# Kernel optimization log

Hardware: AMD Instinct MI355X
Metric: run time of the kernel (lower is better)

Reference implementation:

```python
import jax, jax.numpy as jnp
import numpy as np

N, E, IN, HID, H, L, G = 20000, 320000, 128, 64, 4, 3, 128

def setup_inputs() -> dict:
    key = jax.random.key(0)
    ks = jax.random.split(key, 14)
    x = jax.random.normal(ks[0], (N, IN), dtype=jnp.float32)
    edge_index = jax.random.randint(ks[1], (2, E), 0, N, dtype=jnp.int64)
    batch = jnp.sort(jax.random.randint(ks[2], (N,), 0, G, dtype=jnp.int64))
    s_in = 1.0 / np.sqrt(IN)
    s_h = 1.0 / np.sqrt(HID)
    lin_W = jax.random.normal(ks[3], (IN, HID), jnp.float32) * s_in
    lin_b = jax.random.normal(ks[4], (HID,), jnp.float32) * 0.02
    Wq = jax.random.normal(ks[5], (L, HID, H * HID), jnp.float32) * s_h
    bq = jax.random.normal(ks[6], (L, H * HID), jnp.float32) * 0.02
    Wk = jax.random.normal(ks[7], (L, HID, H * HID), jnp.float32) * s_h
    bk = jax.random.normal(ks[8], (L, H * HID), jnp.float32) * 0.02
    Wv = jax.random.normal(ks[9], (L, HID, H * HID), jnp.float32) * s_h
    bv = jax.random.normal(ks[10], (L, H * HID), jnp.float32) * 0.02
    Ws = jax.random.normal(ks[11], (L, HID, HID), jnp.float32) * s_h
    bs = jax.random.normal(ks[12], (L, HID), jnp.float32) * 0.02
    return {"x": x, "edge_index": edge_index, "batch": batch,
            "lin_W": lin_W, "lin_b": lin_b, "Wq": Wq, "bq": bq,
            "Wk": Wk, "bk": bk, "Wv": Wv, "bv": bv, "Ws": Ws, "bs": bs}

def _transformer_conv(h, src, dst, Wq, bq, Wk, bk, Wv, bv, Ws, bs):
    # PyG TransformerConv(hid, hid, heads=H, concat=False), beta=False, root_weight=True
    n = h.shape[0]
    C = HID  # per-head dim
    q = (h @ Wq + bq).reshape(n, H, C)
    k = (h @ Wk + bk).reshape(n, H, C)
    v = (h @ Wv + bv).reshape(n, H, C)
    # per-edge attention logits: q_i . k_j / sqrt(C), i=dst (target), j=src
    alpha = jnp.einsum('ehc,ehc->eh', q[dst], k[src]) * (1.0 / np.sqrt(C))  # [E,H]
    # segment softmax over edges grouped by target node
    amax = jax.ops.segment_max(alpha, dst, num_segments=n)  # [N,H]
    amax = jnp.where(jnp.isfinite(amax), amax, 0.0)
    ex = jnp.exp(alpha - amax[dst])
    denom = jax.ops.segment_sum(ex, dst, num_segments=n)
    a = ex / jnp.maximum(denom[dst], 1e-16)  # [E,H]
    msg = a[:, :, None] * v[src]  # [E,H,C]
    agg = jax.ops.segment_sum(msg.reshape(-1, H * C), dst, num_segments=n)
    out = agg.reshape(n, H, C).mean(axis=1)  # concat=False -> head mean
    return out + h @ Ws + bs  # root/skip connection

def reference(x, edge_index, batch, lin_W, lin_b, Wq, bq, Wk, bk, Wv, bv, Ws, bs):
    src, dst = edge_index[0], edge_index[1]
    h = x @ lin_W + lin_b  # [N, HID]; dropout inactive in eval
    for l in range(L):
        h = jax.nn.relu(_transformer_conv(h, src, dst, Wq[l], bq[l], Wk[l], bk[l],
                                          Wv[l], bv[l], Ws[l], bs[l]))
    # global_add_pool: sum node features per graph
    return jax.ops.segment_sum(h, batch, num_segments=G)  # [G, HID]
```

## Files before the change

### kernel.cpp

```cpp
#include <hip/hip_runtime.h>
#include <math.h>

#define N_NODES 20000
#define N_EDGES 320000
#define DIM_IN 128
#define HID 64
#define HEADS 4
#define LAYERS 3
#define GRAPHS 128
#define QKVS 832
#define QSS 320

typedef unsigned short ushort;
typedef ushort ushort8 __attribute__((ext_vector_type(8)));

__device__ __forceinline__ float bf2f(ushort u) {
    return __uint_as_float(((unsigned int)u) << 16);
}
__device__ __forceinline__ ushort f2bf(float f) {
    unsigned int b = __float_as_uint(f);
    return (ushort)((b + 0x7FFFu + ((b >> 16) & 1u)) >> 16);
}


__global__ void zero_kernel(int* __restrict__ p, int n) {
    int i = blockIdx.x * 256 + threadIdx.x;
    if (i < n) p[i] = 0;
}

__global__ void hist_kernel(const int* __restrict__ dst, int* __restrict__ counts, int n) {
    int e = blockIdx.x * 256 + threadIdx.x;
    if (e < n) atomicAdd(&counts[dst[e]], 1);
}

__global__ __launch_bounds__(1024) void scan_kernel(const int* __restrict__ counts,
                                                    int* __restrict__ offs,
                                                    int* __restrict__ cursor, int n) {
    __shared__ int wsum[16];
    __shared__ int wpre[17];
    int tid = threadIdx.x;
    int wave = tid >> 6, lane = tid & 63;
    int base = 0;
    int nchunks = (n + 1023) / 1024;
    for (int chunk = 0; chunk < nchunks; ++chunk) {
        int i = chunk * 1024 + tid;
        int v = (i < n) ? counts[i] : 0;
        int s = v;
#pragma unroll
        for (int off = 1; off < 64; off <<= 1) {
            int t = __shfl_up(s, off);
            if (lane >= off) s += t;
        }
        if (lane == 63) wsum[wave] = s;
        __syncthreads();
        if (tid < 16) {
            int w = wsum[tid];
            int ws = w;
#pragma unroll
            for (int off = 1; off < 16; off <<= 1) {
                int t = __shfl_up(ws, off);
                if (lane >= off) ws += t;
            }
            wpre[tid] = ws - w;
            if (tid == 15) wpre[16] = ws;
        }
        __syncthreads();
        int excl = base + (s - v) + wpre[wave];
        if (i < n) { offs[i] = excl; cursor[i] = excl; }
        base += wpre[16];
        __syncthreads();
    }
    if (tid == 0) offs[n] = base;
}

__global__ void scatter_kernel(const int* __restrict__ src, const int* __restrict__ dst,
                               int* __restrict__ cursor, int* __restrict__ csr, int n) {
    int e = blockIdx.x * 256 + threadIdx.x;
    if (e < n) {
        int d = dst[e];
        int pos = atomicAdd(&cursor[d], 1);
        csr[pos] = src[e];
    }
}


__global__ __launch_bounds__(256) void lin_kernel(const float* __restrict__ x,
                                                  const float* __restrict__ W,
                                                  const float* __restrict__ b,
                                                  float* __restrict__ h0) {
    __shared__ float xt[32][DIM_IN];
    int tx = threadIdx.x;
    int row0 = blockIdx.x * 32;
    for (int idx = tx; idx < 32 * DIM_IN; idx += 256) {
        int r = idx / DIM_IN, c = idx % DIM_IN;
        xt[r][c] = x[(size_t)(row0 + r) * DIM_IN + c];
    }
    __syncthreads();
    int col = tx & 63;
    int sub = tx >> 6;
    float acc[8];
#pragma unroll
    for (int r = 0; r < 8; ++r) acc[r] = 0.f;
    for (int k = 0; k < DIM_IN; k += 4) {
        float w0 = W[k * HID + col];
        float w1 = W[(k + 1) * HID + col];
        float w2 = W[(k + 2) * HID + col];
        float w3 = W[(k + 3) * HID + col];
#pragma unroll
        for (int r = 0; r < 8; ++r) {
            const float4 hv = *(const float4*)&xt[r * 4 + sub][k];
            acc[r] += hv.x * w0 + hv.y * w1 + hv.z * w2 + hv.w * w3;
        }
    }
    float bias = b[col];
#pragma unroll
    for (int r = 0; r < 8; ++r) {
        int row = row0 + r * 4 + sub;
        h0[(size_t)row * HID + col] = acc[r] + bias;
    }
}


__global__ __launch_bounds__(256) void proj_kernel(const float* __restrict__ h,
                                                   const float* __restrict__ Wq, const float* __restrict__ bq,
                                                   const float* __restrict__ Wk, const float* __restrict__ bk,
                                                   const float* __restrict__ Wv, const float* __restrict__ bv,
                                                   const float* __restrict__ Ws, const float* __restrict__ bs,
                                                   float* __restrict__ qs,
                                                   ushort* __restrict__ kvpack) {
    __shared__ float ht[16][HID];
    int tx = threadIdx.x;
    int row0 = blockIdx.x * 16;
    for (int idx = tx; idx < 16 * HID; idx += 256) {
        ht[idx >> 6][idx & 63] = h[(size_t)(row0 + (idx >> 6)) * HID + (idx & 63)];
    }
    __syncthreads();
    int j = blockIdx.y * 256 + tx;
    if (j >= QKVS) return;
    const float* W; int ld; float bias;
    if (j < 256)      { W = Wq + j;         ld = 256; bias = bq[j]; }
    else if (j < 512) { W = Wk + (j - 256); ld = 256; bias = bk[j - 256]; }
    else if (j < 768) { W = Wv + (j - 512); ld = 256; bias = bv[j - 512]; }
    else              { W = Ws + (j - 768); ld = 64;  bias = bs[j - 768]; }
    float acc[16];
#pragma unroll
    for (int r = 0; r < 16; ++r) acc[r] = 0.f;
    for (int k = 0; k < HID; k += 4) {
        float w0 = W[(size_t)k * ld];
        float w1 = W[(size_t)(k + 1) * ld];
        float w2 = W[(size_t)(k + 2) * ld];
        float w3 = W[(size_t)(k + 3) * ld];
#pragma unroll
        for (int r = 0; r < 16; ++r) {
            const float4 hv = *(const float4*)&ht[r][k];
            acc[r] += hv.x * w0 + hv.y * w1 + hv.z * w2 + hv.w * w3;
        }
    }
    if (j < 256) {
#pragma unroll
        for (int r = 0; r < 16; ++r)
            qs[(size_t)(row0 + r) * QSS + j] = acc[r] + bias;
    } else if (j < 768) {
        int ck = j - 256;
        int isv = ck >> 8;
        int ch = ck & 255;
        int hh = ch >> 6, c = ch & 63;
        int pos = ((hh * 16 + (c >> 2)) * 8) + isv * 4 + (c & 3);
#pragma unroll
        for (int r = 0; r < 16; ++r)
            kvpack[(size_t)(row0 + r) * 512 + pos] = f2bf(acc[r] + bias);
    } else {
#pragma unroll
        for (int r = 0; r < 16; ++r)
            qs[(size_t)(row0 + r) * QSS + 256 + (j - 768)] = acc[r] + bias;
    }
}


__global__ __launch_bounds__(256) void edge_kernel(const float* __restrict__ qs,
                                                   const ushort8* __restrict__ kvp,
                                                   const int* __restrict__ offs,
                                                   const int* __restrict__ csr,
                                                   float* __restrict__ hout) {
    int wave = threadIdx.x >> 6;
    int lane = threadIdx.x & 63;
    int node = blockIdx.x * 4 + wave;
    if (node >= N_NODES) return;
    int hh = lane >> 4;
    int cb = (lane & 15) * 4;

    const float* nb = qs + (size_t)node * QSS;
    float4 q = *(const float4*)(nb + hh * 64 + cb);

    float m = -INFINITY, l = 0.f;
    float4 acc = make_float4(0.f, 0.f, 0.f, 0.f);

    int e0 = offs[node], e1 = offs[node + 1];
    int cnt = e1 - e0;

    ushort8 cur = (ushort8)(0);
    ushort8 nxt = (ushort8)(0);
    if (cnt > 0) cur = kvp[(size_t)csr[e0] * 64 + lane];
    if (cnt > 1) nxt = kvp[(size_t)csr[e0 + 1] * 64 + lane];

    for (int i = 0; i < cnt; ++i) {
        ushort8 u = cur;
        cur = nxt;
        if (i + 2 < cnt) nxt = kvp[(size_t)csr[e0 + i + 2] * 64 + lane];

        float p = q.x * bf2f(u[0]) + q.y * bf2f(u[1]) + q.z * bf2f(u[2]) + q.w * bf2f(u[3]);
        p += __shfl_xor(p, 1);
        p += __shfl_xor(p, 2);
        p += __shfl_xor(p, 4);
        p += __shfl_xor(p, 8);
        float alpha = p * 0.125f;
        float nm = fmaxf(m, alpha);
        float sc = __expf(m - nm);
        float pe = __expf(alpha - nm);
        l = l * sc + pe;
        acc.x = acc.x * sc + pe * bf2f(u[4]);
        acc.y = acc.y * sc + pe * bf2f(u[5]);
        acc.z = acc.z * sc + pe * bf2f(u[6]);
        acc.w = acc.w * sc + pe * bf2f(u[7]);
        m = nm;
    }

    float inv = (l > 0.f) ? (1.f / l) : 0.f;
    float4 r;
    r.x = acc.x * inv;
    r.y = acc.y * inv;
    r.z = acc.z * inv;
    r.w = acc.w * inv;
    r.x += __shfl_xor(r.x, 16); r.x += __shfl_xor(r.x, 32);
    r.y += __shfl_xor(r.y, 16); r.y += __shfl_xor(r.y, 32);
    r.z += __shfl_xor(r.z, 16); r.z += __shfl_xor(r.z, 32);
    r.w += __shfl_xor(r.w, 16); r.w += __shfl_xor(r.w, 32);

    if (hh == 0) {
        float4 s = *(const float4*)(nb + 256 + cb);
        float4 o;
        o.x = fmaxf(r.x * 0.25f + s.x, 0.f);
        o.y = fmaxf(r.y * 0.25f + s.y, 0.f);
        o.z = fmaxf(r.z * 0.25f + s.z, 0.f);
        o.w = fmaxf(r.w * 0.25f + s.w, 0.f);
        *(float4*)(hout + (size_t)node * HID + cb) = o;
    }
}


__global__ __launch_bounds__(256) void pool_kernel(const float* __restrict__ h,
                                                   const int* __restrict__ batch,
                                                   float* __restrict__ out) {
    int g = blockIdx.x;
    int lo = 0, hi = N_NODES;
    while (lo < hi) { int mid = (lo + hi) >> 1; if (batch[mid] < g) lo = mid + 1; else hi = mid; }
    int start = lo;
    hi = N_NODES;
    while (lo < hi) { int mid = (lo + hi) >> 1; if (batch[mid] < g + 1) lo = mid + 1; else hi = mid; }
    int end = lo;
    int c = threadIdx.x & 63;
    int sub = threadIdx.x >> 6;
    float acc = 0.f;
    for (int i = start + sub; i < end; i += 4) acc += h[(size_t)i * HID + c];
    __shared__ float lds[4][64];
    lds[sub][c] = acc;
    __syncthreads();
    if (sub == 0) out[g * HID + c] = lds[0][c] + lds[1][c] + lds[2][c] + lds[3][c];
}


extern "C" void kernel_launch(void* const* d_in, const int* in_sizes, int n_in,
                              void* d_out, int out_size, void* d_ws, size_t ws_size,
                              hipStream_t stream) {
    const float* x    = (const float*)d_in[0];
    const int*   edge = (const int*)d_in[1];
    const int*   batch= (const int*)d_in[2];
    const float* linW = (const float*)d_in[3];
    const float* linb = (const float*)d_in[4];
    const float* Wq   = (const float*)d_in[5];
    const float* bq   = (const float*)d_in[6];
    const float* Wk   = (const float*)d_in[7];
    const float* bk   = (const float*)d_in[8];
    const float* Wv   = (const float*)d_in[9];
    const float* bv   = (const float*)d_in[10];
    const float* Ws   = (const float*)d_in[11];
    const float* bs   = (const float*)d_in[12];
    float* out = (float*)d_out;

    const int* src = edge;
    const int* dst = edge + N_EDGES;

    float* h0  = (float*)d_ws;
    float* h1  = h0 + (size_t)N_NODES * HID;
    float* qs  = h1 + (size_t)N_NODES * HID;
    ushort* kvpack = (ushort*)(qs + (size_t)N_NODES * QSS);
    int* counts = (int*)(kvpack + (size_t)N_NODES * 512);
    int* offs   = counts + N_NODES;
    int* cursor = offs + N_NODES + 1;
    int* csr    = cursor + N_NODES;

    zero_kernel<<<(N_NODES + 255) / 256, 256, 0, stream>>>(counts, N_NODES);
    hist_kernel<<<(N_EDGES + 255) / 256, 256, 0, stream>>>(dst, counts, N_EDGES);
    scan_kernel<<<1, 1024, 0, stream>>>(counts, offs, cursor, N_NODES);
    scatter_kernel<<<(N_EDGES + 255) / 256, 256, 0, stream>>>(src, dst, cursor, csr, N_EDGES);

    lin_kernel<<<N_NODES / 32, 256, 0, stream>>>(x, linW, linb, h0);

    float* hc = h0;
    float* hn = h1;
    for (int l = 0; l < LAYERS; ++l) {
        dim3 pg(N_NODES / 16, 4);
        proj_kernel<<<pg, 256, 0, stream>>>(hc,
            Wq + (size_t)l * HID * 256, bq + (size_t)l * 256,
            Wk + (size_t)l * HID * 256, bk + (size_t)l * 256,
            Wv + (size_t)l * HID * 256, bv + (size_t)l * 256,
            Ws + (size_t)l * HID * 64,  bs + (size_t)l * 64,
            qs, kvpack);
        edge_kernel<<<N_NODES / 4, 256, 0, stream>>>(qs, (const ushort8*)kvpack, offs, csr, hn);
        float* t = hc; hc = hn; hn = t;
    }

    pool_kernel<<<GRAPHS, 256, 0, stream>>>(hc, batch, out);
}
```

Before: 486.4 us.

## Parallelize CSR offset scan and merge projection column groups into one block

```diff
diff --git a/kernel.cpp b/kernel.cpp
--- a/kernel.cpp
+++ b/kernel.cpp
@@ -8,7 +8,6 @@
 #define HEADS 4
 #define LAYERS 3
 #define GRAPHS 128
-#define QKVS 832
 #define QSS 320
 
 typedef unsigned short ushort;
@@ -23,54 +22,63 @@
 }
 
 
-__global__ void zero_kernel(int* __restrict__ p, int n) {
-    int i = blockIdx.x * 256 + threadIdx.x;
-    if (i < n) p[i] = 0;
-}
-
 __global__ void hist_kernel(const int* __restrict__ dst, int* __restrict__ counts, int n) {
     int e = blockIdx.x * 256 + threadIdx.x;
     if (e < n) atomicAdd(&counts[dst[e]], 1);
 }
 
-__global__ __launch_bounds__(1024) void scan_kernel(const int* __restrict__ counts,
-                                                    int* __restrict__ offs,
-                                                    int* __restrict__ cursor, int n) {
-    __shared__ int wsum[16];
-    __shared__ int wpre[17];
+__global__ __launch_bounds__(256) void blocksum_kernel(const int* __restrict__ counts,
+                                                       int* __restrict__ bsum, int n) {
+    int i = blockIdx.x * 256 + threadIdx.x;
+    int v = (i < n) ? counts[i] : 0;
+    int lane = threadIdx.x & 63, wave = threadIdx.x >> 6;
+#pragma unroll
+    for (int off = 32; off >= 1; off >>= 1) v += __shfl_xor(v, off);
+    __shared__ int ws[4];
+    if (lane == 0) ws[wave] = v;
+    __syncthreads();
+    if (threadIdx.x == 0) bsum[blockIdx.x] = ws[0] + ws[1] + ws[2] + ws[3];
+}
+
+__global__ __launch_bounds__(128) void scanb_kernel(const int* __restrict__ bsum,
+                                                    int* __restrict__ bexcl, int nb) {
     int tid = threadIdx.x;
-    int wave = tid >> 6, lane = tid & 63;
-    int base = 0;
-    int nchunks = (n + 1023) / 1024;
-    for (int chunk = 0; chunk < nchunks; ++chunk) {
-        int i = chunk * 1024 + tid;
-        int v = (i < n) ? counts[i] : 0;
-        int s = v;
-#pragma unroll
-        for (int off = 1; off < 64; off <<= 1) {
-            int t = __shfl_up(s, off);
-            if (lane >= off) s += t;
-        }
-        if (lane == 63) wsum[wave] = s;
-        __syncthreads();
-        if (tid < 16) {
-            int w = wsum[tid];
-            int ws = w;
-#pragma unroll
-            for (int off = 1; off < 16; off <<= 1) {
-                int t = __shfl_up(ws, off);
-                if (lane >= off) ws += t;
-            }
-            wpre[tid] = ws - w;
-            if (tid == 15) wpre[16] = ws;
-        }
-        __syncthreads();
-        int excl = base + (s - v) + wpre[wave];
-        if (i < n) { offs[i] = excl; cursor[i] = excl; }
-        base += wpre[16];
-        __syncthreads();
-    }
-    if (tid == 0) offs[n] = base;
+    int v = (tid < nb) ? bsum[tid] : 0;
+    int lane = tid & 63, wave = tid >> 6;
+    int s = v;
+#pragma unroll
+    for (int off = 1; off < 64; off <<= 1) {
+        int t = __shfl_up(s, off);
+        if (lane >= off) s += t;
+    }
+    __shared__ int w0sum;
+    if (tid == 63) w0sum = s;
+    __syncthreads();
+    int excl = s - v + (wave ? w0sum : 0);
+    if (tid < nb) bexcl[tid] = excl;
+}
+
+__global__ __launch_bounds__(256) void expand_kernel(const int* __restrict__ counts,
+                                                     const int* __restrict__ bexcl,
+                                                     int* __restrict__ offs,
+                                                     int* __restrict__ cursor, int n) {
+    int i = blockIdx.x * 256 + threadIdx.x;
+    int v = (i < n) ? counts[i] : 0;
+    int lane = threadIdx.x & 63, wave = threadIdx.x >> 6;
+    int s = v;
+#pragma unroll
+    for (int off = 1; off < 64; off <<= 1) {
+        int t = __shfl_up(s, off);
+        if (lane >= off) s += t;
+    }
+    __shared__ int wsum[4];
+    if (lane == 63) wsum[wave] = s;
+    __syncthreads();
+    int add = bexcl[blockIdx.x];
+    for (int w = 0; w < wave; ++w) add += wsum[w];
+    int excl = add + s - v;
+    if (i < n) { offs[i] = excl; cursor[i] = excl; }
+    if (i == 0) offs[n] = N_EDGES;
 }
 
 __global__ void scatter_kernel(const int* __restrict__ src, const int* __restrict__ dst,
@@ -135,44 +143,63 @@
         ht[idx >> 6][idx & 63] = h[(size_t)(row0 + (idx >> 6)) * HID + (idx & 63)];
     }
     __syncthreads();
-    int j = blockIdx.y * 256 + tx;
-    if (j >= QKVS) return;
-    const float* W; int ld; float bias;
-    if (j < 256)      { W = Wq + j;         ld = 256; bias = bq[j]; }
-    else if (j < 512) { W = Wk + (j - 256); ld = 256; bias = bk[j - 256]; }
-    else if (j < 768) { W = Wv + (j - 512); ld = 256; bias = bv[j - 512]; }
-    else              { W = Ws + (j - 768); ld = 64;  bias = bs[j - 768]; }
-    float acc[16];
-#pragma unroll
-    for (int r = 0; r < 16; ++r) acc[r] = 0.f;
+    const bool do_s = (tx < 64);
+    float accq[16], acck[16], accv[16], accs[16];
+#pragma unroll
+    for (int r = 0; r < 16; ++r) { accq[r] = 0.f; acck[r] = 0.f; accv[r] = 0.f; accs[r] = 0.f; }
+
     for (int k = 0; k < HID; k += 4) {
-        float w0 = W[(size_t)k * ld];
-        float w1 = W[(size_t)(k + 1) * ld];
-        float w2 = W[(size_t)(k + 2) * ld];
-        float w3 = W[(size_t)(k + 3) * ld];
+        float wq0 = Wq[(size_t)k * 256 + tx];
+        float wq1 = Wq[(size_t)(k + 1) * 256 + tx];
+        float wq2 = Wq[(size_t)(k + 2) * 256 + tx];
+        float wq3 = Wq[(size_t)(k + 3) * 256 + tx];
+        float wk0 = Wk[(size_t)k * 256 + tx];
+        float wk1 = Wk[(size_t)(k + 1) * 256 + tx];
+        float wk2 = Wk[(size_t)(k + 2) * 256 + tx];
+        float wk3 = Wk[(size_t)(k + 3) * 256 + tx];
+        float wv0 = Wv[(size_t)k * 256 + tx];
+        float wv1 = Wv[(size_t)(k + 1) * 256 + tx];
+        float wv2 = Wv[(size_t)(k + 2) * 256 + tx];
+        float wv3 = Wv[(size_t)(k + 3) * 256 + tx];
+        float ws0 = 0.f, ws1 = 0.f, ws2 = 0.f, ws3 = 0.f;
+        if (do_s) {
+            ws0 = Ws[(size_t)k * 64 + tx];
+            ws1 = Ws[(size_t)(k + 1) * 64 + tx];
+            ws2 = Ws[(size_t)(k + 2) * 64 + tx];
+            ws3 = Ws[(size_t)(k + 3) * 64 + tx];
+        }
 #pragma unroll
         for (int r = 0; r < 16; ++r) {
             const float4 hv = *(const float4*)&ht[r][k];
-            acc[r] += hv.x * w0 + hv.y * w1 + hv.z * w2 + hv.w * w3;
+            accq[r] += hv.x * wq0 + hv.y * wq1 + hv.z * wq2 + hv.w * wq3;
+            acck[r] += hv.x * wk0 + hv.y * wk1 + hv.z * wk2 + hv.w * wk3;
+            accv[r] += hv.x * wv0 + hv.y * wv1 + hv.z * wv2 + hv.w * wv3;
         }
-    }
-    if (j < 256) {
+        if (do_s) {
+#pragma unroll
+            for (int r = 0; r < 16; ++r) {
+                const float4 hv = *(const float4*)&ht[r][k];
+                accs[r] += hv.x * ws0 + hv.y * ws1 + hv.z * ws2 + hv.w * ws3;
+            }
+        }
+    }
+
+    float biasq = bq[tx], biask = bk[tx], biasv = bv[tx];
+    int hh = tx >> 6, c = tx & 63;
+    int posk = (hh * 16 + (c >> 2)) * 8 + (c & 3);
+    int posv = posk + 4;
+#pragma unroll
+    for (int r = 0; r < 16; ++r) {
+        size_t row = row0 + r;
+        qs[row * QSS + tx] = accq[r] + biasq;
+        kvpack[row * 512 + posk] = f2bf(acck[r] + biask);
+        kvpack[row * 512 + posv] = f2bf(accv[r] + biasv);
+    }
+    if (do_s) {
+        float biass = bs[tx];
 #pragma unroll
         for (int r = 0; r < 16; ++r)
-            qs[(size_t)(row0 + r) * QSS + j] = acc[r] + bias;
-    } else if (j < 768) {
-        int ck = j - 256;
-        int isv = ck >> 8;
-        int ch = ck & 255;
-        int hh = ch >> 6, c = ch & 63;
-        int pos = ((hh * 16 + (c >> 2)) * 8) + isv * 4 + (c & 3);
-#pragma unroll
-        for (int r = 0; r < 16; ++r)
-            kvpack[(size_t)(row0 + r) * 512 + pos] = f2bf(acc[r] + bias);
-    } else {
-#pragma unroll
-        for (int r = 0; r < 16; ++r)
-            qs[(size_t)(row0 + r) * QSS + 256 + (j - 768)] = acc[r] + bias;
+            qs[(size_t)(row0 + r) * QSS + 256 + tx] = accs[r] + biass;
     }
 }
 
@@ -298,10 +325,16 @@
     int* offs   = counts + N_NODES;
     int* cursor = offs + N_NODES + 1;
     int* csr    = cursor + N_NODES;
-
-    zero_kernel<<<(N_NODES + 255) / 256, 256, 0, stream>>>(counts, N_NODES);
+    int* bsum   = csr + N_EDGES;
+    int* bexcl  = bsum + 128;
+
+    const int NB = (N_NODES + 255) / 256;
+
+    hipMemsetAsync(counts, 0, N_NODES * sizeof(int), stream);
     hist_kernel<<<(N_EDGES + 255) / 256, 256, 0, stream>>>(dst, counts, N_EDGES);
-    scan_kernel<<<1, 1024, 0, stream>>>(counts, offs, cursor, N_NODES);
+    blocksum_kernel<<<NB, 256, 0, stream>>>(counts, bsum, N_NODES);
+    scanb_kernel<<<1, 128, 0, stream>>>(bsum, bexcl, NB);
+    expand_kernel<<<NB, 256, 0, stream>>>(counts, bexcl, offs, cursor, N_NODES);
     scatter_kernel<<<(N_EDGES + 255) / 256, 256, 0, stream>>>(src, dst, cursor, csr, N_EDGES);
 
     lin_kernel<<<N_NODES / 32, 256, 0, stream>>>(x, linW, linb, h0);
@@ -309,8 +342,7 @@
     float* hc = h0;
     float* hn = h1;
     for (int l = 0; l < LAYERS; ++l) {
-        dim3 pg(N_NODES / 16, 4);
-        proj_kernel<<<pg, 256, 0, stream>>>(hc,
+        proj_kernel<<<N_NODES / 16, 256, 0, stream>>>(hc,
             Wq + (size_t)l * HID * 256, bq + (size_t)l * 256,
             Wk + (size_t)l * HID * 256, bk + (size_t)l * 256,
             Wv + (size_t)l * HID * 256, bv + (size_t)l * 256,
```

Result: faster. 445.9 us (-8.3%).
